# Kernel optimization log

Hardware: AMD Instinct MI355X
Metric: run time of the kernel (lower is better)

Reference implementation:

```python
import jax, jax.numpy as jnp
import numpy as np

B, T, V, E, H = 4, 2048, 50257, 1024, 16
D = E // H  # head dim = 64

def _ln(x, g, b, eps=1e-5):
    mu = jnp.mean(x, axis=-1, keepdims=True)
    var = jnp.var(x, axis=-1, keepdims=True)
    return (x - mu) * jax.lax.rsqrt(var + eps) * g + b

def setup_inputs() -> dict:
    key = jax.random.key(0)
    ks = jax.random.split(key, 20)
    s = 0.02
    return {
        "ids": jax.random.randint(ks[0], (B, T), 0, V),
        "wte": jax.random.normal(ks[1], (V, E), jnp.float32) * s,
        "wpe": jax.random.normal(ks[2], (T, E), jnp.float32) * s,
        "wq": jax.random.normal(ks[3], (H, E, D), jnp.float32) * s,
        "wk": jax.random.normal(ks[4], (H, E, D), jnp.float32) * s,
        "wv": jax.random.normal(ks[5], (H, E, D), jnp.float32) * s,
        "bq": jnp.zeros((H, D), jnp.float32),
        "bk": jnp.zeros((H, D), jnp.float32),
        "bv": jnp.zeros((H, D), jnp.float32),
        "wproj": jax.random.normal(ks[6], (E, E), jnp.float32) * s,
        "bproj": jnp.zeros((E,), jnp.float32),
        "ln1_g": jnp.ones((E,), jnp.float32),
        "ln1_b": jnp.zeros((E,), jnp.float32),
        "ln2_g": jnp.ones((E,), jnp.float32),
        "ln2_b": jnp.zeros((E,), jnp.float32),
        "w_fc": jax.random.normal(ks[7], (E, 4 * E), jnp.float32) * s,
        "b_fc": jnp.zeros((4 * E,), jnp.float32),
        "w_out": jax.random.normal(ks[8], (4 * E, E), jnp.float32) * s,
        "b_out": jnp.zeros((E,), jnp.float32),
    }

def reference(ids, wte, wpe, wq, wk, wv, bq, bk, bv, wproj, bproj,
              ln1_g, ln1_b, ln2_g, ln2_b, w_fc, b_fc, w_out, b_out):
    t = ids.shape[1]
    x = wte[ids] + wpe[:t]                      # [B,T,E]
    # --- attention (all heads batched; faithful per-head math) ---
    h = _ln(x, ln1_g, ln1_b)
    q = jnp.einsum('btc,hcd->bhtd', h, wq) + bq[None, :, None, :]
    k = jnp.einsum('btc,hcd->bhtd', h, wk) + bk[None, :, None, :]
    v = jnp.einsum('btc,hcd->bhtd', h, wv) + bv[None, :, None, :]
    scores = jnp.einsum('bhtd,bhsd->bhts', q, k) * (1.0 / np.sqrt(D))
    causal = jnp.tril(jnp.ones((t, t), bool))
    scores = jnp.where(causal, scores, -jnp.inf)
    attn = jax.nn.softmax(scores, axis=-1)      # dropout = identity (eval)
    o = jnp.einsum('bhts,bhsd->bhtd', attn, v)
    o = jnp.transpose(o, (0, 2, 1, 3)).reshape(x.shape[0], t, E)  # concat heads
    x = x + o @ wproj + bproj
    # --- MLP ---
    h2 = _ln(x, ln2_g, ln2_b)
    m = jax.nn.gelu(h2 @ w_fc + b_fc, approximate=False) @ w_out + b_out
    return x + m
```

## Files before the change

kernel.cpp:

```cpp
#include <hip/hip_runtime.h>
#include <math.h>

#define BB 4
#define TT 2048
#define EE 1024
#define HH 16
#define DD 64
#define MM (BB*TT)

typedef unsigned short u16;
typedef __bf16 bf16x8 __attribute__((ext_vector_type(8)));
typedef float  f32x4  __attribute__((ext_vector_type(4)));

__device__ inline float bf2f(u16 u){ union{unsigned int i; float f;} v; v.i=((unsigned int)u)<<16; return v.f; }
__device__ inline u16 f2bf(float f){ union{float f; unsigned int i;} v; v.f=f; return (u16)((v.i + 0x7fffu + ((v.i>>16)&1u))>>16); }
__device__ inline u16 f2bf_trunc(float f){ union{float f; unsigned int i;} v; v.f=f; return (u16)(v.i>>16); }

__device__ inline void gload_lds16(const void* g, void* l){
  __builtin_amdgcn_global_load_lds((__attribute__((address_space(1))) void*)g,
                                   (__attribute__((address_space(3))) void*)l, 16, 0, 0);
}

__global__ __launch_bounds__(256) void transpose_tile(
    const float* __restrict__ W, u16* __restrict__ WT, int N, int K)
{
    __shared__ float t[32][33];
    const int n0 = blockIdx.x*32, k0 = blockIdx.y*32;
    const int tx = threadIdx.x, ty = threadIdx.y;
    #pragma unroll
    for (int j=0;j<4;j++)
        t[ty + j*8][tx] = W[(size_t)(k0 + ty + j*8)*N + n0 + tx];
    __syncthreads();
    #pragma unroll
    for (int j=0;j<4;j++)
        WT[(size_t)(n0 + ty + j*8)*K + k0 + tx] = f2bf(t[tx][ty + j*8]);
}

__global__ __launch_bounds__(256) void transpose_v(
    const u16* __restrict__ V, u16* __restrict__ VT)
{
    __shared__ u16 t[32][34];
    const int bh = blockIdx.z;
    const int t0 = blockIdx.x*32;
    const int d0 = blockIdx.y*32;
    const int tx = threadIdx.x, ty = threadIdx.y;
    const u16* Vb = V + (size_t)bh*TT*DD;
    u16* VTb = VT + (size_t)bh*TT*DD;
    #pragma unroll
    for (int j=0;j<4;j++)
        t[ty+j*8][tx] = Vb[(size_t)(t0+ty+j*8)*DD + d0+tx];
    __syncthreads();
    #pragma unroll
    for (int j=0;j<4;j++)
        VTb[(size_t)(d0+ty+j*8)*TT + t0+tx] = t[tx][ty+j*8];
}

__global__ __launch_bounds__(256) void repack_qkv_tiled(
    const float* __restrict__ wq, const float* __restrict__ wk, const float* __restrict__ wv,
    u16* __restrict__ WT)
{
    __shared__ float t[32][33];
    const int z = blockIdx.z, which = z>>4, hh = z&15;
    const int d0 = blockIdx.x*32, c0 = blockIdx.y*32;
    const int tx = threadIdx.x, ty = threadIdx.y;
    const float* w = which==0 ? wq : (which==1 ? wk : wv);
    #pragma unroll
    for (int j=0;j<4;j++)
        t[ty + j*8][tx] = w[((size_t)hh*EE + c0 + ty + j*8)*DD + d0 + tx];
    __syncthreads();
    #pragma unroll
    for (int j=0;j<4;j++)
        WT[(size_t)(which*1024 + hh*64 + d0 + ty + j*8)*1024 + c0 + tx] = f2bf(t[tx][ty + j*8]);
}

__global__ __launch_bounds__(256) void copy_bias_qkv(
    const float* __restrict__ bq, const float* __restrict__ bk, const float* __restrict__ bv,
    float* __restrict__ bias)
{
    int i = blockIdx.x*256 + threadIdx.x;
    const float* b = i<1024 ? bq : (i<2048 ? bk : bv);
    bias[i] = b[i & 1023];
}

__global__ __launch_bounds__(256) void embed_ln1(
    const int* __restrict__ ids, const float* __restrict__ wte, const float* __restrict__ wpe,
    const float* __restrict__ g, const float* __restrict__ b,
    float* __restrict__ x_out, u16* __restrict__ h_out)
{
    const int token = blockIdx.x;
    const int t = token & (TT-1);
    const int id = ids[token];
    const int tid = threadIdx.x;
    float vals[4]; float s=0.f, s2=0.f;
    #pragma unroll
    for (int i=0;i<4;i++){
        int e = tid + i*256;
        float v = wte[(size_t)id*EE + e] + wpe[(size_t)t*EE + e];
        vals[i]=v; s+=v; s2+=v*v;
    }
    for (int off=32; off>=1; off>>=1){ s += __shfl_xor(s,off); s2 += __shfl_xor(s2,off); }
    __shared__ float red[8];
    int wave=tid>>6, lane=tid&63;
    if (lane==0){ red[wave]=s; red[4+wave]=s2; }
    __syncthreads();
    s = red[0]+red[1]+red[2]+red[3];
    s2 = red[4]+red[5]+red[6]+red[7];
    float mu = s*(1.f/EE);
    float var = s2*(1.f/EE) - mu*mu;
    float rstd = rsqrtf(var + 1e-5f);
    #pragma unroll
    for (int i=0;i<4;i++){
        int e = tid + i*256; float v = vals[i];
        x_out[(size_t)token*EE + e] = v;
        h_out[(size_t)token*EE + e] = f2bf((v-mu)*rstd*g[e] + b[e]);
    }
}

__global__ __launch_bounds__(256) void ln_fwd(
    const float* __restrict__ xin, const float* __restrict__ g, const float* __restrict__ b,
    u16* __restrict__ hout)
{
    const int token = blockIdx.x;
    const int tid = threadIdx.x;
    float vals[4]; float s=0.f, s2=0.f;
    #pragma unroll
    for (int i=0;i<4;i++){
        int e = tid + i*256;
        float v = xin[(size_t)token*EE + e];
        vals[i]=v; s+=v; s2+=v*v;
    }
    for (int off=32; off>=1; off>>=1){ s += __shfl_xor(s,off); s2 += __shfl_xor(s2,off); }
    __shared__ float red[8];
    int wave=tid>>6, lane=tid&63;
    if (lane==0){ red[wave]=s; red[4+wave]=s2; }
    __syncthreads();
    s = red[0]+red[1]+red[2]+red[3];
    s2 = red[4]+red[5]+red[6]+red[7];
    float mu = s*(1.f/EE);
    float var = s2*(1.f/EE) - mu*mu;
    float rstd = rsqrtf(var + 1e-5f);
    #pragma unroll
    for (int i=0;i<4;i++){
        int e = tid + i*256; float v = vals[i];
        hout[(size_t)token*EE + e] = f2bf((v-mu)*rstd*g[e] + b[e]);
    }
}


#define VMCNTW(N) asm volatile("s_waitcnt vmcnt(" #N ")" ::: "memory")
#define LGKMW(N)  asm volatile("s_waitcnt lgkmcnt(" #N ")" ::: "memory")
#define SCHEDB()  __builtin_amdgcn_sched_barrier(0)
#define BAR()     { SCHEDB(); __builtin_amdgcn_s_barrier(); SCHEDB(); }

__device__ __forceinline__ bf16x8 fld(const u16* base, int row, int j){
    return *(const bf16x8*)&base[(row<<6) + ((j ^ (row&7))<<3)];
}

template<int MODE>
__global__ __launch_bounds__(512,2) void gemm256(
    const u16* __restrict__ A, const u16* __restrict__ BT, const float* __restrict__ bias,
    float* CoutF, const float* resid, u16* __restrict__ CoutH,
    u16* __restrict__ q_out, u16* __restrict__ k_out, u16* __restrict__ v_out,
    int Ndim, int Kdim)
{
    __shared__ alignas(16) u16 As[2][256*64];
    __shared__ alignas(16) u16 Bs[2][256*64];
    const int tid = threadIdx.x, wave = tid>>6, lane = tid&63;
    const int quad = (lane>>4)&3, l16 = lane&15;
    const int wr = wave>>2, wc = wave&3;

    const int nwg = gridDim.x;
    const int chunk = nwg>>3;
    int id = blockIdx.x;
    id = (id&7)*chunk + (id>>3);
    const int m0 = (id & 31) << 8;
    const int n0 = (id >> 5) << 8;

    const int rS = tid>>3;
    const int jS = (tid&7) ^ (rS&7);
    const size_t off0   = (size_t)rS*Kdim + (size_t)(jS<<3);
    const size_t ofs64K = (size_t)64*Kdim;
    const u16* pA = A  + (size_t)m0*Kdim;
    const u16* pB = BT + (size_t)n0*Kdim;

#define STAGE(ARR, GP, BUF, H, KT)                                             \
  { const u16* _g = (GP) + (size_t)((H)*128)*Kdim + (size_t)(KT)*64 + off0;    \
    gload_lds16(_g,          &ARR[BUF][(H)*8192 + wave*512]);                  \
    gload_lds16(_g + ofs64K, &ARR[BUF][(H)*8192 + 4096 + wave*512]); }

    STAGE(As, pA, 0, 0, 0);
    STAGE(Bs, pB, 0, 0, 0);
    STAGE(Bs, pB, 0, 1, 0);
    STAGE(As, pA, 0, 1, 0);
    STAGE(As, pA, 1, 0, 1);
    STAGE(Bs, pB, 1, 0, 1);
    STAGE(Bs, pB, 1, 1, 1);

    f32x4 acc[8][4];
    const f32x4 zf = {0.f,0.f,0.f,0.f};
    #pragma unroll
    for (int i=0;i<8;i++)
        #pragma unroll
        for (int j=0;j<4;j++) acc[i][j]=zf;

    bf16x8 af[4][2], bfr[4][2];

#define LDA(HROW)                                                              \
  { _Pragma("unroll") for (int mt=0; mt<4; mt++)                               \
    { _Pragma("unroll") for (int kh=0; kh<2; kh++)                             \
        af[mt][kh] = fld(Ab, (HROW) + (wr<<6) + (mt<<4) + l16, kh*4+quad); } }
#define LDB(HROW, NTB)                                                         \
  { _Pragma("unroll") for (int nt=0; nt<2; nt++)                               \
    { _Pragma("unroll") for (int kh=0; kh<2; kh++)                             \
        bfr[(NTB)+nt][kh] = fld(Bb, (HROW) + (wc<<5) + (nt<<4) + l16, kh*4+quad); } }
#define MFMA16(MT0, NT0)                                                       \
  __builtin_amdgcn_s_setprio(1);                                               \
  { _Pragma("unroll") for (int mt=0; mt<4; mt++)                               \
    { _Pragma("unroll") for (int nt=0; nt<2; nt++)                             \
      { _Pragma("unroll") for (int kh=0; kh<2; kh++)                           \
          acc[(MT0)+mt][(NT0)+nt] = __builtin_amdgcn_mfma_f32_16x16x32_bf16(   \
              af[mt][kh], bfr[(NT0)+nt][kh], acc[(MT0)+mt][(NT0)+nt], 0,0,0);  \
      } } }                                                                    \
  __builtin_amdgcn_s_setprio(0);

    VMCNTW(6);
    BAR();

    const int NT = Kdim>>6;
    for (int kt=0; kt<NT; ++kt){
        const int b = kt&1;
        const u16* Ab = As[b];
        const u16* Bb = Bs[b];
        LDA(0); LDB(0,0);
        if (kt+1 < NT) STAGE(As, pA, b^1, 1, kt+1);
        LGKMW(8);
        BAR(); LGKMW(0); SCHEDB();
        MFMA16(0,0);
        BAR();
        LDB(128,2);
        if (kt+2 < NT) STAGE(As, pA, b, 0, kt+2);
        BAR(); LGKMW(0); SCHEDB();
        MFMA16(0,2);
        BAR();
        LDA(128);
        if (kt+2 < NT) STAGE(Bs, pB, b, 0, kt+2);
        BAR(); LGKMW(0); SCHEDB();
        MFMA16(4,2);
        BAR();
        if (kt+2 < NT) STAGE(Bs, pB, b, 1, kt+2);
        BAR();
        MFMA16(4,0);
        if (kt+2 < NT)      { VMCNTW(6); }
        else if (kt+1 < NT) { VMCNTW(0); }
        BAR();
    }
#undef STAGE
#undef LDA
#undef LDB
#undef MFMA16

    #pragma unroll
    for (int mt=0; mt<8; mt++){
        const int mrow = m0 + ((mt<4) ? (wr<<6)+(mt<<4) : 128+(wr<<6)+((mt-4)<<4)) + (quad<<2);
        #pragma unroll
        for (int nt=0; nt<4; nt++){
            const int n = n0 + ((nt<2) ? (wc<<5)+(nt<<4) : 128+(wc<<5)+((nt-2)<<4)) + l16;
            #pragma unroll
            for (int r=0;r<4;r++){
                const int m = mrow + r;
                float v = acc[mt][nt][r] + bias[n];
                if (MODE==0){
                    int which = n>>10, hd = n&1023, hh = hd>>6, d = hd&63;
                    u16* dst = which==0 ? q_out : (which==1 ? k_out : v_out);
                    int bb = m>>11, t = m&(TT-1);
                    dst[(((size_t)(bb*HH+hh)*TT + t)<<6) + d] = f2bf(v);
                } else if (MODE==1){
                    size_t idx = (size_t)m*Ndim + n;
                    CoutF[idx] = resid[idx] + v;
                } else {
                    size_t idx = (size_t)m*Ndim + n;
                    CoutH[idx] = f2bf(0.5f*v*(1.0f + erff(v*0.70710678118f)));
                }
            }
        }
    }
}

__device__ __forceinline__ void attn_proc_tile(
    int kt, int q0, int quad, int l16,
    const u16* Ks, const u16* Vs, u16* Psw,
    const bf16x8 (&qf)[2][2], f32x4 (&oacc)[2][4], float (&lsum)[2][4])
{
    if (kt > ((q0+31)>>6)) return;
    const f32x4 zf = {0.f,0.f,0.f,0.f};
    f32x4 a[2][4];
    #pragma unroll
    for (int m=0;m<2;m++)
        #pragma unroll
        for (int st=0;st<4;st++) a[m][st]=zf;
    #pragma unroll
    for (int h2=0;h2<2;h2++){
        #pragma unroll
        for (int st=0;st<4;st++){
            const int s = st*16 + l16;
            const int jc = h2*4 + quad;
            bf16x8 kf = *(const bf16x8*)&Ks[s*64 + (jc ^ (s&7))*8];
            #pragma unroll
            for (int m=0;m<2;m++)
                a[m][st] = __builtin_amdgcn_mfma_f32_16x16x32_bf16(qf[m][h2], kf, a[m][st], 0,0,0);
        }
    }
    const bool needMask = (kt*64 + 63 > q0);
    #pragma unroll
    for (int m=0;m<2;m++){
        const int q0m = q0 + m*16;
        #pragma unroll
        for (int st=0;st<4;st++){
            #pragma unroll
            for (int r=0;r<4;r++){
                float p = exp2f(fminf(a[m][st][r]*0.1803369f, 40.f));
                if (needMask){
                    const int qrow = q0m + quad*4 + r;
                    const int s = kt*64 + st*16 + l16;
                    if (s > qrow) p = 0.f;
                }
                lsum[m][r] += p;
                const int ql = m*16 + quad*4 + r;
                const int sc3 = st*2 + (l16>>3);
                Psw[ql*64 + (sc3 ^ (ql&7))*8 + (l16&7)] = f2bf_trunc(p);
            }
        }
    }
    #pragma unroll
    for (int kh=0; kh<2; kh++){
        const int jc = kh*4 + quad;
        bf16x8 pf[2];
        #pragma unroll
        for (int m=0;m<2;m++){
            const int ql16 = m*16 + l16;
            pf[m] = *(const bf16x8*)&Psw[ql16*64 + (jc ^ (ql16&7))*8];
        }
        #pragma unroll
        for (int dt=0; dt<4; dt++){
            const int d = dt*16 + l16;
            bf16x8 vf = *(const bf16x8*)&Vs[d*64 + (jc ^ (d&7))*8];
            #pragma unroll
            for (int m=0;m<2;m++)
                oacc[m][dt] = __builtin_amdgcn_mfma_f32_16x16x32_bf16(pf[m], vf, oacc[m][dt], 0,0,0);
        }
    }
}

__global__ __launch_bounds__(256,2) void attn_kernel(
    const u16* __restrict__ Q, const u16* __restrict__ K, const u16* __restrict__ VT,
    u16* __restrict__ O)
{
    __shared__ u16 Ks[64*64];
    __shared__ u16 Vs[64*64];
    __shared__ u16 Ps[4*2048];
    const int tid = threadIdx.x, wave = tid>>6, lane = tid&63;
    const int quad = lane>>4, l16 = lane&15;
    const int id = blockIdx.x;
    const int bh   = (id&7) | ((id>>6)<<3);
    const int pair = (id>>3)&7;
    const int qtA = pair, qtB = 15-pair;
    const size_t base = (size_t)bh*TT*DD;
    const u16* Qb = Q + base;
    const u16* Kb = K + base;
    const u16* VTb = VT + base;
    const int qA0 = qtA*128 + wave*32;
    const int qB0 = qtB*128 + wave*32;
    u16* Psw = &Ps[wave*2048];

    bf16x8 qfA[2][2], qfB[2][2];
    #pragma unroll
    for (int m=0;m<2;m++)
        #pragma unroll
        for (int h2=0;h2<2;h2++){
            qfA[m][h2] = *(const bf16x8*)&Qb[(size_t)(qA0+m*16+l16)*DD + h2*32 + quad*8];
            qfB[m][h2] = *(const bf16x8*)&Qb[(size_t)(qB0+m*16+l16)*DD + h2*32 + quad*8];
        }

    const f32x4 zf = {0.f,0.f,0.f,0.f};
    f32x4 oaccA[2][4], oaccB[2][4];
    float lsumA[2][4], lsumB[2][4];
    #pragma unroll
    for (int m=0;m<2;m++){
        #pragma unroll
        for (int dt=0;dt<4;dt++){ oaccA[m][dt]=zf; oaccB[m][dt]=zf; }
        #pragma unroll
        for (int r=0;r<4;r++){ lsumA[m][r]=0.f; lsumB[m][r]=0.f; }
    }

    const int ktMax = 31 - 2*pair;

    const int c0 = wave*64 + lane, c1 = 256 + wave*64 + lane;
    const int r0 = c0>>3, j0 = (c0&7) ^ (r0&7);
    const int r1 = c1>>3, j1 = (c1&7) ^ (r1&7);

    for (int kt=0; kt<=ktMax; kt++){
        __syncthreads();
        {
            const int s0 = kt*64;
            gload_lds16(Kb  + (size_t)(s0+r0)*DD + j0*8, &Ks[wave*512]);
            gload_lds16(Kb  + (size_t)(s0+r1)*DD + j1*8, &Ks[(4+wave)*512]);
            gload_lds16(VTb + (size_t)r0*TT + s0 + j0*8, &Vs[wave*512]);
            gload_lds16(VTb + (size_t)r1*TT + s0 + j1*8, &Vs[(4+wave)*512]);
        }
        __syncthreads();
        attn_proc_tile(kt, qB0, quad, l16, Ks, Vs, Psw, qfB, oaccB, lsumB);
        attn_proc_tile(kt, qA0, quad, l16, Ks, Vs, Psw, qfA, oaccA, lsumA);
    }

    #pragma unroll
    for (int off=1; off<16; off<<=1)
        #pragma unroll
        for (int m=0;m<2;m++)
            #pragma unroll
            for (int r=0;r<4;r++){
                lsumA[m][r] += __shfl_xor(lsumA[m][r], off);
                lsumB[m][r] += __shfl_xor(lsumB[m][r], off);
            }

    const int bb = bh>>4, hh = bh&15;
    #pragma unroll
    for (int m=0;m<2;m++)
        #pragma unroll
        for (int dt=0;dt<4;dt++)
            #pragma unroll
            for (int r=0;r<4;r++){
                int t = qA0 + m*16 + quad*4 + r;
                O[(size_t)(bb*TT + t)*EE + hh*64 + dt*16 + l16] = f2bf(oaccA[m][dt][r] / lsumA[m][r]);
                t = qB0 + m*16 + quad*4 + r;
                O[(size_t)(bb*TT + t)*EE + hh*64 + dt*16 + l16] = f2bf(oaccB[m][dt][r] / lsumB[m][r]);
            }
}

extern "C" void kernel_launch(void* const* d_in, const int* in_sizes, int n_in,
                              void* d_out, int out_size, void* d_ws, size_t ws_size,
                              hipStream_t stream)
{
    (void)in_sizes; (void)n_in; (void)out_size; (void)ws_size;
    const int*   ids  = (const int*)d_in[0];
    const float* wte  = (const float*)d_in[1];
    const float* wpe  = (const float*)d_in[2];
    const float* wq   = (const float*)d_in[3];
    const float* wk   = (const float*)d_in[4];
    const float* wv   = (const float*)d_in[5];
    const float* bq   = (const float*)d_in[6];
    const float* bk   = (const float*)d_in[7];
    const float* bv   = (const float*)d_in[8];
    const float* wproj= (const float*)d_in[9];
    const float* bproj= (const float*)d_in[10];
    const float* ln1g = (const float*)d_in[11];
    const float* ln1b = (const float*)d_in[12];
    const float* ln2g = (const float*)d_in[13];
    const float* ln2b = (const float*)d_in[14];
    const float* wfc  = (const float*)d_in[15];
    const float* bfc  = (const float*)d_in[16];
    const float* wout = (const float*)d_in[17];
    const float* bout = (const float*)d_in[18];

    const size_t MTOK = (size_t)MM*EE;
    char* p = (char*)d_ws;
    float* x    = (float*)p;  p += MTOK*sizeof(float);
    u16*  h     = (u16*)p;    p += MTOK*sizeof(u16);
    u16*  Qb    = (u16*)p;    p += MTOK*sizeof(u16);
    u16*  Kb    = (u16*)p;    p += MTOK*sizeof(u16);
    u16*  Vb    = (u16*)p;    p += MTOK*sizeof(u16);
    u16*  Ob    = (u16*)p;    p += MTOK*sizeof(u16);
    u16*  fcact = Qb;
    u16*  VTv   = h;
    u16*  WqkvT = (u16*)p;    p += (size_t)3072*1024*sizeof(u16);
    float* biasq= (float*)p;  p += 3072*sizeof(float);
    u16*  wprojT= (u16*)p;    p += (size_t)1024*1024*sizeof(u16);
    u16*  wfcT  = (u16*)p;    p += (size_t)4096*1024*sizeof(u16);
    u16*  woutT = (u16*)p;    p += (size_t)1024*4096*sizeof(u16);
    float* out  = (float*)d_out;

    repack_qkv_tiled<<<dim3(2,32,48),dim3(32,8),0,stream>>>(wq,wk,wv,WqkvT);
    copy_bias_qkv<<<12,256,0,stream>>>(bq,bk,bv,biasq);
    transpose_tile<<<dim3(32,32), dim3(32,8),0,stream>>>(wproj, wprojT, 1024, 1024);
    transpose_tile<<<dim3(128,32),dim3(32,8),0,stream>>>(wfc,   wfcT,   4096, 1024);
    transpose_tile<<<dim3(32,128),dim3(32,8),0,stream>>>(wout,  woutT,  1024, 4096);
    embed_ln1<<<MM,256,0,stream>>>(ids, wte, wpe, ln1g, ln1b, x, h);
    gemm256<0><<<32*12,512,0,stream>>>(h, WqkvT, biasq, nullptr,nullptr,nullptr, Qb,Kb,Vb, 3072, 1024);
    transpose_v<<<dim3(64,2,64),dim3(32,8),0,stream>>>(Vb, VTv);
    attn_kernel<<<512,256,0,stream>>>(Qb,Kb,VTv,Ob);
    gemm256<1><<<32*4,512,0,stream>>>(Ob, wprojT, bproj, x, x, nullptr, nullptr,nullptr,nullptr, 1024, 1024);
    ln_fwd<<<MM,256,0,stream>>>(x, ln2g, ln2b, h);
    gemm256<2><<<32*16,512,0,stream>>>(h, wfcT, bfc, nullptr,nullptr, fcact, nullptr,nullptr,nullptr, 4096, 1024);
    gemm256<1><<<32*4,512,0,stream>>>(fcact, woutT, bout, out, x, nullptr, nullptr,nullptr,nullptr, 1024, 4096);
}
```

Measured before the change: 793.3 us.

## Add 128x256-tile GEMM variant for QKV and N=1024 projections

Adds a gemm128 kernel with 128x256 output tiles (half the M-tile of gemm256) and a matching double-buffered LDS pipeline, then uses it for the QKV, attention-projection and MLP-output GEMMs. The N=1024 GEMMs previously launched only 128 workgroups on a 256-CU device; smaller tiles double the grid so more CUs are busy. The cost is lower operand reuse per tile and more global/LDS traffic per flop. The FC GEMM keeps the 256x256 kernel.

```diff
diff --git a/kernel.cpp b/kernel.cpp
--- a/kernel.cpp
+++ b/kernel.cpp
@@ -145,7 +145,6 @@
         hout[(size_t)token*EE + e] = f2bf((v-mu)*rstd*g[e] + b[e]);
     }
 }
-
 
 #define VMCNTW(N) asm volatile("s_waitcnt vmcnt(" #N ")" ::: "memory")
 #define LGKMW(N)  asm volatile("s_waitcnt lgkmcnt(" #N ")" ::: "memory")
@@ -265,6 +264,128 @@
         #pragma unroll
         for (int nt=0; nt<4; nt++){
             const int n = n0 + ((nt<2) ? (wc<<5)+(nt<<4) : 128+(wc<<5)+((nt-2)<<4)) + l16;
+            #pragma unroll
+            for (int r=0;r<4;r++){
+                const int m = mrow + r;
+                float v = acc[mt][nt][r] + bias[n];
+                if (MODE==0){
+                    int which = n>>10, hd = n&1023, hh = hd>>6, d = hd&63;
+                    u16* dst = which==0 ? q_out : (which==1 ? k_out : v_out);
+                    int bb = m>>11, t = m&(TT-1);
+                    dst[(((size_t)(bb*HH+hh)*TT + t)<<6) + d] = f2bf(v);
+                } else if (MODE==1){
+                    size_t idx = (size_t)m*Ndim + n;
+                    CoutF[idx] = resid[idx] + v;
+                } else {
+                    size_t idx = (size_t)m*Ndim + n;
+                    CoutH[idx] = f2bf(0.5f*v*(1.0f + erff(v*0.70710678118f)));
+                }
+            }
+        }
+    }
+}
+
+template<int MODE>
+__global__ __launch_bounds__(512,2) void gemm128(
+    const u16* __restrict__ A, const u16* __restrict__ BT, const float* __restrict__ bias,
+    float* CoutF, const float* resid, u16* __restrict__ CoutH,
+    u16* __restrict__ q_out, u16* __restrict__ k_out, u16* __restrict__ v_out,
+    int Ndim, int Kdim)
+{
+    __shared__ alignas(16) u16 As[2][128*64];
+    __shared__ alignas(16) u16 Bs[2][256*64];
+    const int tid = threadIdx.x, wave = tid>>6, lane = tid&63;
+    const int quad = (lane>>4)&3, l16 = lane&15;
+    const int wr = wave>>2, wc = wave&3;
+
+    const int nwg = gridDim.x;
+    const int chunk = nwg>>3;
+    int id = blockIdx.x;
+    id = (id&7)*chunk + (id>>3);
+    const int nT = Ndim>>8;
+    const int n0 = (id % nT) << 8;
+    const int m0 = (id / nT) << 7;
+
+    const int rS = tid>>3;
+    const int jS = (tid&7) ^ (rS&7);
+    const size_t off0 = (size_t)rS*Kdim + (size_t)(jS<<3);
+    const u16* pA = A  + (size_t)m0*Kdim;
+    const u16* pB = BT + (size_t)n0*Kdim;
+
+#define STG(ARR, GP, BUF, U, KT)                                               \
+    gload_lds16((GP) + (size_t)((U)*64)*Kdim + (size_t)(KT)*64 + off0,         \
+                &ARR[BUF][(U)*4096 + wave*512]);
+
+    STG(As,pA,0,0,0); STG(As,pA,0,1,0);
+    STG(Bs,pB,0,0,0); STG(Bs,pB,0,1,0); STG(Bs,pB,0,2,0); STG(Bs,pB,0,3,0);
+    STG(As,pA,1,0,1); STG(As,pA,1,1,1);
+    STG(Bs,pB,1,0,1); STG(Bs,pB,1,1,1); STG(Bs,pB,1,2,1); STG(Bs,pB,1,3,1);
+
+    f32x4 acc[4][4];
+    const f32x4 zf = {0.f,0.f,0.f,0.f};
+    #pragma unroll
+    for (int i=0;i<4;i++)
+        #pragma unroll
+        for (int j=0;j<4;j++) acc[i][j]=zf;
+
+    bf16x8 af[4][2], bfr[2][2];
+
+#define LDA8()                                                                 \
+  { _Pragma("unroll") for (int mt=0; mt<4; mt++)                               \
+    { _Pragma("unroll") for (int kh=0; kh<2; kh++)                             \
+        af[mt][kh] = fld(Ab, (wr<<6) + (mt<<4) + l16, kh*4+quad); } }
+#define LDB4(NTB)                                                              \
+  { _Pragma("unroll") for (int nt=0; nt<2; nt++)                               \
+    { _Pragma("unroll") for (int kh=0; kh<2; kh++)                             \
+        bfr[nt][kh] = fld(Bb, (wc<<6) + (((NTB)+nt)<<4) + l16, kh*4+quad); } }
+#define MFMA16B(NT0)                                                           \
+  __builtin_amdgcn_s_setprio(1);                                               \
+  { _Pragma("unroll") for (int mt=0; mt<4; mt++)                               \
+    { _Pragma("unroll") for (int nt=0; nt<2; nt++)                             \
+      { _Pragma("unroll") for (int kh=0; kh<2; kh++)                           \
+          acc[mt][(NT0)+nt] = __builtin_amdgcn_mfma_f32_16x16x32_bf16(         \
+              af[mt][kh], bfr[nt][kh], acc[mt][(NT0)+nt], 0,0,0);              \
+      } } }                                                                    \
+  __builtin_amdgcn_s_setprio(0);
+
+    VMCNTW(6);
+    BAR();
+
+    const int NT = Kdim>>6;
+    for (int kt=0; kt<NT; ++kt){
+        const int b = kt&1;
+        const u16* Ab = As[b];
+        const u16* Bb = Bs[b];
+        LDA8(); LDB4(0);
+        LGKMW(8);
+        BAR(); LGKMW(0); SCHEDB();
+        MFMA16B(0);
+        BAR();
+        LDB4(2);
+        if (kt+2 < NT){
+            STG(As,pA,b,0,kt+2); STG(As,pA,b,1,kt+2);
+            STG(Bs,pB,b,0,kt+2); STG(Bs,pB,b,1,kt+2);
+        }
+        BAR(); LGKMW(0); SCHEDB();
+        MFMA16B(2);
+        BAR();
+        if (kt+2 < NT){
+            STG(Bs,pB,b,2,kt+2); STG(Bs,pB,b,3,kt+2);
+            VMCNTW(6);
+        } else if (kt+1 < NT) { VMCNTW(0); }
+        BAR();
+    }
+#undef STG
+#undef LDA8
+#undef LDB4
+#undef MFMA16B
+
+    #pragma unroll
+    for (int mt=0; mt<4; mt++){
+        const int mrow = m0 + (wr<<6) + (mt<<4) + (quad<<2);
+        #pragma unroll
+        for (int nt=0; nt<4; nt++){
+            const int n = n0 + (wc<<6) + (nt<<4) + l16;
             #pragma unroll
             for (int r=0;r<4;r++){
                 const int m = mrow + r;
@@ -484,11 +605,11 @@
     transpose_tile<<<dim3(128,32),dim3(32,8),0,stream>>>(wfc,   wfcT,   4096, 1024);
     transpose_tile<<<dim3(32,128),dim3(32,8),0,stream>>>(wout,  woutT,  1024, 4096);
     embed_ln1<<<MM,256,0,stream>>>(ids, wte, wpe, ln1g, ln1b, x, h);
-    gemm256<0><<<32*12,512,0,stream>>>(h, WqkvT, biasq, nullptr,nullptr,nullptr, Qb,Kb,Vb, 3072, 1024);
+    gemm128<0><<<768,512,0,stream>>>(h, WqkvT, biasq, nullptr,nullptr,nullptr, Qb,Kb,Vb, 3072, 1024);
     transpose_v<<<dim3(64,2,64),dim3(32,8),0,stream>>>(Vb, VTv);
     attn_kernel<<<512,256,0,stream>>>(Qb,Kb,VTv,Ob);
-    gemm256<1><<<32*4,512,0,stream>>>(Ob, wprojT, bproj, x, x, nullptr, nullptr,nullptr,nullptr, 1024, 1024);
+    gemm128<1><<<256,512,0,stream>>>(Ob, wprojT, bproj, x, x, nullptr, nullptr,nullptr,nullptr, 1024, 1024);
     ln_fwd<<<MM,256,0,stream>>>(x, ln2g, ln2b, h);
-    gemm256<2><<<32*16,512,0,stream>>>(h, wfcT, bfc, nullptr,nullptr, fcact, nullptr,nullptr,nullptr, 4096, 1024);
-    gemm256<1><<<32*4,512,0,stream>>>(fcact, woutT, bout, out, x, nullptr, nullptr,nullptr,nullptr, 1024, 4096);
-}
+    gemm256<2><<<512,512,0,stream>>>(h, wfcT, bfc, nullptr,nullptr, fcact, nullptr,nullptr,nullptr, 4096, 1024);
+    gemm128<1><<<256,512,0,stream>>>(fcact, woutT, bout, out, x, nullptr, nullptr,nullptr,nullptr, 1024, 4096);
+}
```

Result: faster. 742.7 us (-6.4%).

## Shrink GEMM tile to 128x256 and double-buffer K/V loads in attention

Applied to the files above, without the earlier changes.

Changes the GEMM from 256x256 to 128x256 output tiles, so each wave now owns a 64x64 output block. Grid counts double, which improves fill on the 256-CU device for the smaller projection GEMMs (128 to 256 blocks). The attention kernel double-buffers its K/V LDS tiles, prefetching the next tile while the current one is processed. It also raises wave priority around the MFMA sections. In exchange, the GEMM gets less A/B reuse per tile and runs fewer MFMAs between barriers, while attention uses more LDS per block.

```diff
diff --git a/kernel.cpp b/kernel.cpp
--- a/kernel.cpp
+++ b/kernel.cpp
@@ -146,7 +146,6 @@
     }
 }
 
-
 #define VMCNTW(N) asm volatile("s_waitcnt vmcnt(" #N ")" ::: "memory")
 #define LGKMW(N)  asm volatile("s_waitcnt lgkmcnt(" #N ")" ::: "memory")
 #define SCHEDB()  __builtin_amdgcn_sched_barrier(0)
@@ -157,13 +156,13 @@
 }
 
 template<int MODE>
-__global__ __launch_bounds__(512,2) void gemm256(
+__global__ __launch_bounds__(512,2) void gemm128(
     const u16* __restrict__ A, const u16* __restrict__ BT, const float* __restrict__ bias,
     float* CoutF, const float* resid, u16* __restrict__ CoutH,
     u16* __restrict__ q_out, u16* __restrict__ k_out, u16* __restrict__ v_out,
     int Ndim, int Kdim)
 {
-    __shared__ alignas(16) u16 As[2][256*64];
+    __shared__ alignas(16) u16 As[2][128*64];
     __shared__ alignas(16) u16 Bs[2][256*64];
     const int tid = threadIdx.x, wave = tid>>6, lane = tid&63;
     const int quad = (lane>>4)&3, l16 = lane&15;
@@ -173,53 +172,49 @@
     const int chunk = nwg>>3;
     int id = blockIdx.x;
     id = (id&7)*chunk + (id>>3);
-    const int m0 = (id & 31) << 8;
-    const int n0 = (id >> 5) << 8;
+    const int nT = Ndim>>8;
+    const int n0 = (id % nT) << 8;
+    const int m0 = (id / nT) << 7;
 
     const int rS = tid>>3;
     const int jS = (tid&7) ^ (rS&7);
-    const size_t off0   = (size_t)rS*Kdim + (size_t)(jS<<3);
-    const size_t ofs64K = (size_t)64*Kdim;
+    const size_t off0 = (size_t)rS*Kdim + (size_t)(jS<<3);
     const u16* pA = A  + (size_t)m0*Kdim;
     const u16* pB = BT + (size_t)n0*Kdim;
 
-#define STAGE(ARR, GP, BUF, H, KT)                                             \
-  { const u16* _g = (GP) + (size_t)((H)*128)*Kdim + (size_t)(KT)*64 + off0;    \
-    gload_lds16(_g,          &ARR[BUF][(H)*8192 + wave*512]);                  \
-    gload_lds16(_g + ofs64K, &ARR[BUF][(H)*8192 + 4096 + wave*512]); }
-
-    STAGE(As, pA, 0, 0, 0);
-    STAGE(Bs, pB, 0, 0, 0);
-    STAGE(Bs, pB, 0, 1, 0);
-    STAGE(As, pA, 0, 1, 0);
-    STAGE(As, pA, 1, 0, 1);
-    STAGE(Bs, pB, 1, 0, 1);
-    STAGE(Bs, pB, 1, 1, 1);
-
-    f32x4 acc[8][4];
+#define STG(ARR, GP, BUF, U, KT)                                               \
+    gload_lds16((GP) + (size_t)((U)*64)*Kdim + (size_t)(KT)*64 + off0,         \
+                &ARR[BUF][(U)*4096 + wave*512]);
+
+    STG(As,pA,0,0,0); STG(As,pA,0,1,0);
+    STG(Bs,pB,0,0,0); STG(Bs,pB,0,1,0); STG(Bs,pB,0,2,0); STG(Bs,pB,0,3,0);
+    STG(As,pA,1,0,1); STG(As,pA,1,1,1);
+    STG(Bs,pB,1,0,1); STG(Bs,pB,1,1,1); STG(Bs,pB,1,2,1); STG(Bs,pB,1,3,1);
+
+    f32x4 acc[4][4];
     const f32x4 zf = {0.f,0.f,0.f,0.f};
     #pragma unroll
-    for (int i=0;i<8;i++)
+    for (int i=0;i<4;i++)
         #pragma unroll
         for (int j=0;j<4;j++) acc[i][j]=zf;
 
-    bf16x8 af[4][2], bfr[4][2];
-
-#define LDA(HROW)                                                              \
+    bf16x8 af[4][2], bfr[2][2];
+
+#define LDA8()                                                                 \
   { _Pragma("unroll") for (int mt=0; mt<4; mt++)                               \
     { _Pragma("unroll") for (int kh=0; kh<2; kh++)                             \
-        af[mt][kh] = fld(Ab, (HROW) + (wr<<6) + (mt<<4) + l16, kh*4+quad); } }
-#define LDB(HROW, NTB)                                                         \
+        af[mt][kh] = fld(Ab, (wr<<6) + (mt<<4) + l16, kh*4+quad); } }
+#define LDB4(NTB)                                                              \
   { _Pragma("unroll") for (int nt=0; nt<2; nt++)                               \
     { _Pragma("unroll") for (int kh=0; kh<2; kh++)                             \
-        bfr[(NTB)+nt][kh] = fld(Bb, (HROW) + (wc<<5) + (nt<<4) + l16, kh*4+quad); } }
-#define MFMA16(MT0, NT0)                                                       \
+        bfr[nt][kh] = fld(Bb, (wc<<6) + (((NTB)+nt)<<4) + l16, kh*4+quad); } }
+#define MFMA16B(NT0)                                                           \
   __builtin_amdgcn_s_setprio(1);                                               \
   { _Pragma("unroll") for (int mt=0; mt<4; mt++)                               \
     { _Pragma("unroll") for (int nt=0; nt<2; nt++)                             \
       { _Pragma("unroll") for (int kh=0; kh<2; kh++)                           \
-          acc[(MT0)+mt][(NT0)+nt] = __builtin_amdgcn_mfma_f32_16x16x32_bf16(   \
-              af[mt][kh], bfr[(NT0)+nt][kh], acc[(MT0)+mt][(NT0)+nt], 0,0,0);  \
+          acc[mt][(NT0)+nt] = __builtin_amdgcn_mfma_f32_16x16x32_bf16(         \
+              af[mt][kh], bfr[nt][kh], acc[mt][(NT0)+nt], 0,0,0);              \
       } } }                                                                    \
   __builtin_amdgcn_s_setprio(0);
 
@@ -231,40 +226,36 @@
         const int b = kt&1;
         const u16* Ab = As[b];
         const u16* Bb = Bs[b];
-        LDA(0); LDB(0,0);
-        if (kt+1 < NT) STAGE(As, pA, b^1, 1, kt+1);
+        LDA8(); LDB4(0);
         LGKMW(8);
         BAR(); LGKMW(0); SCHEDB();
-        MFMA16(0,0);
+        MFMA16B(0);
         BAR();
-        LDB(128,2);
-        if (kt+2 < NT) STAGE(As, pA, b, 0, kt+2);
+        LDB4(2);
+        if (kt+2 < NT){
+            STG(As,pA,b,0,kt+2); STG(As,pA,b,1,kt+2);
+            STG(Bs,pB,b,0,kt+2); STG(Bs,pB,b,1,kt+2);
+        }
         BAR(); LGKMW(0); SCHEDB();
-        MFMA16(0,2);
+        MFMA16B(2);
         BAR();
-        LDA(128);
-        if (kt+2 < NT) STAGE(Bs, pB, b, 0, kt+2);
-        BAR(); LGKMW(0); SCHEDB();
-        MFMA16(4,2);
+        if (kt+2 < NT){
+            STG(Bs,pB,b,2,kt+2); STG(Bs,pB,b,3,kt+2);
+            VMCNTW(6);
+        } else if (kt+1 < NT) { VMCNTW(0); }
         BAR();
-        if (kt+2 < NT) STAGE(Bs, pB, b, 1, kt+2);
-        BAR();
-        MFMA16(4,0);
-        if (kt+2 < NT)      { VMCNTW(6); }
-        else if (kt+1 < NT) { VMCNTW(0); }
-        BAR();
-    }
-#undef STAGE
-#undef LDA
-#undef LDB
-#undef MFMA16
-
-    #pragma unroll
-    for (int mt=0; mt<8; mt++){
-        const int mrow = m0 + ((mt<4) ? (wr<<6)+(mt<<4) : 128+(wr<<6)+((mt-4)<<4)) + (quad<<2);
+    }
+#undef STG
+#undef LDA8
+#undef LDB4
+#undef MFMA16B
+
+    #pragma unroll
+    for (int mt=0; mt<4; mt++){
+        const int mrow = m0 + (wr<<6) + (mt<<4) + (quad<<2);
         #pragma unroll
         for (int nt=0; nt<4; nt++){
-            const int n = n0 + ((nt<2) ? (wc<<5)+(nt<<4) : 128+(wc<<5)+((nt-2)<<4)) + l16;
+            const int n = n0 + (wc<<6) + (nt<<4) + l16;
             #pragma unroll
             for (int r=0;r<4;r++){
                 const int m = mrow + r;
@@ -298,6 +289,7 @@
     for (int m=0;m<2;m++)
         #pragma unroll
         for (int st=0;st<4;st++) a[m][st]=zf;
+    __builtin_amdgcn_s_setprio(1);
     #pragma unroll
     for (int h2=0;h2<2;h2++){
         #pragma unroll
@@ -310,6 +302,7 @@
                 a[m][st] = __builtin_amdgcn_mfma_f32_16x16x32_bf16(qf[m][h2], kf, a[m][st], 0,0,0);
         }
     }
+    __builtin_amdgcn_s_setprio(0);
     const bool needMask = (kt*64 + 63 > q0);
     #pragma unroll
     for (int m=0;m<2;m++){
@@ -331,6 +324,7 @@
             }
         }
     }
+    __builtin_amdgcn_s_setprio(1);
     #pragma unroll
     for (int kh=0; kh<2; kh++){
         const int jc = kh*4 + quad;
@@ -349,14 +343,15 @@
                 oacc[m][dt] = __builtin_amdgcn_mfma_f32_16x16x32_bf16(pf[m], vf, oacc[m][dt], 0,0,0);
         }
     }
+    __builtin_amdgcn_s_setprio(0);
 }
 
 __global__ __launch_bounds__(256,2) void attn_kernel(
     const u16* __restrict__ Q, const u16* __restrict__ K, const u16* __restrict__ VT,
     u16* __restrict__ O)
 {
-    __shared__ u16 Ks[64*64];
-    __shared__ u16 Vs[64*64];
+    __shared__ u16 Ks[2][64*64];
+    __shared__ u16 Vs[2][64*64];
     __shared__ u16 Ps[4*2048];
     const int tid = threadIdx.x, wave = tid>>6, lane = tid&63;
     const int quad = lane>>4, l16 = lane&15;
@@ -380,6 +375,7 @@
             qfA[m][h2] = *(const bf16x8*)&Qb[(size_t)(qA0+m*16+l16)*DD + h2*32 + quad*8];
             qfB[m][h2] = *(const bf16x8*)&Qb[(size_t)(qB0+m*16+l16)*DD + h2*32 + quad*8];
         }
+    VMCNTW(0); SCHEDB();
 
     const f32x4 zf = {0.f,0.f,0.f,0.f};
     f32x4 oaccA[2][4], oaccB[2][4];
@@ -398,19 +394,24 @@
     const int r0 = c0>>3, j0 = (c0&7) ^ (r0&7);
     const int r1 = c1>>3, j1 = (c1&7) ^ (r1&7);
 
+#define STAGEKV(KT, BUF)                                                       \
+  { const int s0 = (KT)*64;                                                    \
+    gload_lds16(Kb  + (size_t)(s0+r0)*DD + j0*8, &Ks[BUF][wave*512]);          \
+    gload_lds16(Kb  + (size_t)(s0+r1)*DD + j1*8, &Ks[BUF][(4+wave)*512]);      \
+    gload_lds16(VTb + (size_t)r0*TT + s0 + j0*8, &Vs[BUF][wave*512]);          \
+    gload_lds16(VTb + (size_t)r1*TT + s0 + j1*8, &Vs[BUF][(4+wave)*512]); }
+
+    STAGEKV(0, 0);
     for (int kt=0; kt<=ktMax; kt++){
-        __syncthreads();
-        {
-            const int s0 = kt*64;
-            gload_lds16(Kb  + (size_t)(s0+r0)*DD + j0*8, &Ks[wave*512]);
-            gload_lds16(Kb  + (size_t)(s0+r1)*DD + j1*8, &Ks[(4+wave)*512]);
-            gload_lds16(VTb + (size_t)r0*TT + s0 + j0*8, &Vs[wave*512]);
-            gload_lds16(VTb + (size_t)r1*TT + s0 + j1*8, &Vs[(4+wave)*512]);
-        }
-        __syncthreads();
-        attn_proc_tile(kt, qB0, quad, l16, Ks, Vs, Psw, qfB, oaccB, lsumB);
-        attn_proc_tile(kt, qA0, quad, l16, Ks, Vs, Psw, qfA, oaccA, lsumA);
-    }
+        const int b = kt&1;
+        if (kt < ktMax){ STAGEKV(kt+1, b^1); VMCNTW(4); }
+        else           { VMCNTW(0); }
+        BAR();
+        attn_proc_tile(kt, qB0, quad, l16, Ks[b], Vs[b], Psw, qfB, oaccB, lsumB);
+        attn_proc_tile(kt, qA0, quad, l16, Ks[b], Vs[b], Psw, qfA, oaccA, lsumA);
+        BAR();
+    }
+#undef STAGEKV
 
     #pragma unroll
     for (int off=1; off<16; off<<=1)
@@ -484,11 +485,11 @@
     transpose_tile<<<dim3(128,32),dim3(32,8),0,stream>>>(wfc,   wfcT,   4096, 1024);
     transpose_tile<<<dim3(32,128),dim3(32,8),0,stream>>>(wout,  woutT,  1024, 4096);
     embed_ln1<<<MM,256,0,stream>>>(ids, wte, wpe, ln1g, ln1b, x, h);
-    gemm256<0><<<32*12,512,0,stream>>>(h, WqkvT, biasq, nullptr,nullptr,nullptr, Qb,Kb,Vb, 3072, 1024);
+    gemm128<0><<<768,512,0,stream>>>(h, WqkvT, biasq, nullptr,nullptr,nullptr, Qb,Kb,Vb, 3072, 1024);
     transpose_v<<<dim3(64,2,64),dim3(32,8),0,stream>>>(Vb, VTv);
     attn_kernel<<<512,256,0,stream>>>(Qb,Kb,VTv,Ob);
-    gemm256<1><<<32*4,512,0,stream>>>(Ob, wprojT, bproj, x, x, nullptr, nullptr,nullptr,nullptr, 1024, 1024);
+    gemm128<1><<<256,512,0,stream>>>(Ob, wprojT, bproj, x, x, nullptr, nullptr,nullptr,nullptr, 1024, 1024);
     ln_fwd<<<MM,256,0,stream>>>(x, ln2g, ln2b, h);
-    gemm256<2><<<32*16,512,0,stream>>>(h, wfcT, bfc, nullptr,nullptr, fcact, nullptr,nullptr,nullptr, 4096, 1024);
-    gemm256<1><<<32*4,512,0,stream>>>(fcact, woutT, bout, out, x, nullptr, nullptr,nullptr,nullptr, 1024, 4096);
-}
+    gemm128<2><<<1024,512,0,stream>>>(h, wfcT, bfc, nullptr,nullptr, fcact, nullptr,nullptr,nullptr, 4096, 1024);
+    gemm128<1><<<256,512,0,stream>>>(fcact, woutT, bout, out, x, nullptr, nullptr,nullptr,nullptr, 1024, 4096);
+}
```

Measured after the change: 762.2 us. -3.9%, faster.
